# Kernel tuning notes

Hardware: AMD Instinct MI355X
Metric: run time of the kernel (lower is better)

Reference implementation:

```python
import jax, jax.numpy as jnp
import numpy as np

S = 16; N = 32768; E = 131072


def _lstm(x, h, c, Wih, Whh, b):
    # PyTorch LSTMCell: gates ordered i, f, g, o
    g = x @ Wih + h @ Whh + b
    i, f, gg, o = jnp.split(g, 4, axis=-1)
    c2 = jax.nn.sigmoid(f) * c + jax.nn.sigmoid(i) * jnp.tanh(gg)
    return jax.nn.sigmoid(o) * jnp.tanh(c2), c2


def setup_inputs() -> dict:
    key = jax.random.key(0)
    ks = jax.random.split(key, 24)
    rn = lambda k, shp, fan: (jax.random.normal(k, shp, jnp.float32) / np.float32(np.sqrt(fan)))
    return {
        'data_nodes': jax.random.normal(ks[0], (S + 1, N, 1), jnp.float32),
        'data_temporalEdges': jax.random.normal(ks[1], (S + 1, N, 2), jnp.float32),
        'data_spatialEdges': jax.random.normal(ks[2], (S + 1, E, 2), jnp.float32),
        'h_nodeRNN': jnp.zeros((N, 128), jnp.float32),
        'c_nodeRNN': jnp.zeros((N, 128), jnp.float32),
        'h_temporalEdgeRNN': jnp.zeros((N, 64), jnp.float32),
        'c_temporalEdgeRNN': jnp.zeros((N, 64), jnp.float32),
        'h_spatialEdgeRNN': jnp.zeros((E, 64), jnp.float32),
        'c_spatialEdgeRNN': jnp.zeros((E, 64), jnp.float32),
        'inc_nodes': jax.random.randint(ks[3], (2 * E,), 0, N),
        't_enc_w': rn(ks[4], (2, 64), 2), 't_enc_b': jnp.zeros((64,), jnp.float32),
        't_Wih': rn(ks[5], (64, 256), 64), 't_Whh': rn(ks[6], (64, 256), 64), 't_b': jnp.zeros((256,), jnp.float32),
        's_enc_w': rn(ks[7], (2, 64), 2), 's_enc_b': jnp.zeros((64,), jnp.float32),
        's_Wih': rn(ks[8], (64, 256), 64), 's_Whh': rn(ks[9], (64, 256), 64), 's_b': jnp.zeros((256,), jnp.float32),
        'n_enc_w': rn(ks[10], (1, 64), 1), 'n_enc_b': jnp.zeros((64,), jnp.float32),
        'ee_w': rn(ks[11], (128, 64), 128), 'ee_b': jnp.zeros((64,), jnp.float32),
        'n_Wih': rn(ks[12], (128, 512), 128), 'n_Whh': rn(ks[13], (128, 512), 128), 'n_b': jnp.zeros((512,), jnp.float32),
        'out_w': rn(ks[14], (128, 1), 128), 'out_b': jnp.zeros((1,), jnp.float32),
    }


def reference(data_nodes, data_temporalEdges, data_spatialEdges,
              h_nodeRNN, c_nodeRNN, h_temporalEdgeRNN, c_temporalEdgeRNN,
              h_spatialEdgeRNN, c_spatialEdgeRNN, inc_nodes,
              t_enc_w, t_enc_b, t_Wih, t_Whh, t_b,
              s_enc_w, s_enc_b, s_Wih, s_Whh, s_b,
              n_enc_w, n_enc_b, ee_w, ee_b, n_Wih, n_Whh, n_b, out_w, out_b):
    n_nodes = h_nodeRNN.shape[0]
    n_edges = h_spatialEdgeRNN.shape[0]
    seq_len = data_nodes.shape[0] - 1
    edge_of_inc = jnp.repeat(jnp.arange(n_edges), 2)  # edge index per incidence

    def step(carry, xs):
        ht, ct, hs, cs, hn, cn = carry
        xt, xsp, xn = xs
        # temporal EdgeRNN (dropout is identity in eval)
        ht, ct = _lstm(jax.nn.relu(xt @ t_enc_w + t_enc_b), ht, ct, t_Wih, t_Whh, t_b)
        # spatial EdgeRNN
        hs, cs = _lstm(jax.nn.relu(xsp @ s_enc_w + s_enc_b), hs, cs, s_Wih, s_Whh, s_b)
        # per-node sum of connected spatial-edge hidden states (segment reduce)
        agg = jax.ops.segment_sum(hs[edge_of_inc], inc_nodes, num_segments=n_nodes)
        h_edge = jnp.concatenate([ht, agg], axis=1)  # [N, 2*edge_rnn]
        # NodeRNN
        enc = jax.nn.relu(xn @ n_enc_w + n_enc_b)
        emb = jax.nn.relu(h_edge @ ee_w + ee_b)
        hn, cn = _lstm(jnp.concatenate([enc, emb], axis=1), hn, cn, n_Wih, n_Whh, n_b)
        out = hn @ out_w + out_b
        return (ht, ct, hs, cs, hn, cn), out

    xs = (data_temporalEdges[:seq_len], data_spatialEdges[:seq_len], data_nodes[:seq_len])
    carry0 = (h_temporalEdgeRNN, c_temporalEdgeRNN, h_spatialEdgeRNN, c_spatialEdgeRNN, h_nodeRNN, c_nodeRNN)
    _, outputs = jax.lax.scan(step, carry0, xs)
    return outputs  # [seq_len, N, node_output_size]
```

## Files before the change

### kernel.cpp

```cpp
#include <hip/hip_runtime.h>
#include <math.h>


#define S_LEN 16
#define NN 32768
#define EE 131072

typedef _Float16 f16;
typedef _Float16 f16x8 __attribute__((ext_vector_type(8)));
typedef float f32x4 __attribute__((ext_vector_type(4)));

__device__ __forceinline__ float fsigmoid(float x) {
    return __builtin_amdgcn_rcpf(1.0f + __builtin_amdgcn_exp2f(-1.44269504f * x));
}
__device__ __forceinline__ float ftanh(float x) {
    const float e = __builtin_amdgcn_exp2f(2.88539008f * x);
    return 1.0f - 2.0f * __builtin_amdgcn_rcpf(e + 1.0f);
}

__device__ __forceinline__ unsigned int pk2(float a, float b) {
    union { f16 h[2]; unsigned int u; } x;
    x.h[0] = (f16)a; x.h[1] = (f16)b;
    return x.u;
}

__device__ __forceinline__ f16x8 ld_frag16(const void* p) {
    union { uint4 v; f16x8 f; } x;
    x.v = *(const uint4*)p;
    return x.f;
}

#define CSWZ(rl) (((((rl) >> 2) & 3) ^ ((rl) & 3)) << 4)

__global__ __launch_bounds__(256) void edge_mega(
    const float* __restrict__ xT, const float* __restrict__ xS,
    const float* __restrict__ t_enc_w, const float* __restrict__ t_enc_b,
    const float* __restrict__ s_enc_w, const float* __restrict__ s_enc_b,
    const f16* __restrict__ WtT, const f16* __restrict__ WtS,
    const float* __restrict__ biasT, const float* __restrict__ biasS,
    f16* __restrict__ htAll, f16* __restrict__ hsAll,
    const float* __restrict__ cInT, const float* __restrict__ cInS,
    float* __restrict__ cOutT, float* __restrict__ cOutS,
    const int nsteps, const int writeC)
{
    constexpr int H = 64, K = 128, KSTEPS = 4, ROWB = 256, TR = 64;
    constexpr int RTN = TR / 16;
    __shared__ __align__(16) char Xls[TR * ROWB];
    __shared__ __align__(16) float cls[TR * H];
    __shared__ __align__(16) f16 hnx[TR * H];

    const int bT = NN / TR;
    const bool isT = (int)blockIdx.x < bT;
    const int row0 = (isT ? blockIdx.x : blockIdx.x - bT) * TR;
    const float* xbase = isT ? xT : xS;
    const size_t xstep = (size_t)(isT ? NN : EE) * 2;
    const float* enc_w = isT ? t_enc_w : s_enc_w;
    const float* enc_b = isT ? t_enc_b : s_enc_b;
    const f16*   Wt    = isT ? WtT : WtS;
    const float* bias  = isT ? biasT : biasS;
    f16* hAll = isT ? htAll : hsAll;
    const size_t hstep = (size_t)(isT ? NN : EE) * 64;
    const float* cIn  = (isT ? cInT : cInS) + (size_t)row0 * H;
    float*       cOut = (isT ? cOutT : cOutS) + (size_t)row0 * H;

    const int t = threadIdx.x;
    const int wv = t >> 6, l = t & 63;
    const int lane15 = l & 15, kgrp = l >> 4;
    const int col = wv * 16 + lane15;

    f16x8 bfrag[4][KSTEPS];
    #pragma unroll
    for (int q = 0; q < 4; ++q) {
        const int colq = q * H + col;
        const f16* bp = Wt + (size_t)colq * K + kgrp * 8;
        #pragma unroll
        for (int ks = 0; ks < KSTEPS; ++ks)
            bfrag[q][ks] = ld_frag16(bp + ks * 32);
    }

    for (int i = t; i < TR * H; i += 256) {
        const int r = i >> 6, j = i & 63;
        cls[(r << 6) + (j ^ CSWZ(r))] = cIn[i];
    }
    {
        const f16* hInit = hAll + (size_t)(nsteps - 1) * hstep + (size_t)row0 * H;
        for (int i = t; i < TR * (H / 4); i += 256) {
            const int r = i / (H / 4), j4 = (i % (H / 4)) * 4;
            const uint2 v = *(const uint2*)&hInit[(size_t)r * H + j4];
            const int byte = r * ROWB + ((H * 2 + j4 * 2) ^ ((r & 7) << 4));
            *(uint2*)(Xls + byte) = v;
        }
    }

    const float bi = bias[0 * H + col];
    const float bf = bias[1 * H + col];
    const float bg = bias[2 * H + col];
    const float bo = bias[3 * H + col];

    float xr0[8], xr1[8];
    {
        const float* xf = xbase;
        #pragma unroll
        for (int k2 = 0; k2 < 8; ++k2) {
            const int r = (t + k2 * 256) >> 5;
            xr0[k2] = xf[(size_t)(row0 + r) * 2 + 0];
            xr1[k2] = xf[(size_t)(row0 + r) * 2 + 1];
        }
    }

    for (int s = 0; s < nsteps; ++s) {
        #pragma unroll
        for (int k2 = 0; k2 < 8; ++k2) {
            const int i = t + k2 * 256;
            const int r = i >> 5, j2 = (i & 31) * 2;
            const float x0 = xr0[k2];
            const float x1 = xr1[k2];
            const float e0 = fmaxf(0.f, fmaf(x0, enc_w[j2],     fmaf(x1, enc_w[H + j2],     enc_b[j2])));
            const float e1 = fmaxf(0.f, fmaf(x0, enc_w[j2 + 1], fmaf(x1, enc_w[H + j2 + 1], enc_b[j2 + 1])));
            const int byte = r * ROWB + ((j2 * 2) ^ ((r & 7) << 4));
            *(unsigned int*)(Xls + byte) = pk2(e0, e1);
        }
        __syncthreads();

        if (s + 1 < nsteps) {
            const float* xf = xbase + (size_t)(s + 1) * xstep;
            #pragma unroll
            for (int k2 = 0; k2 < 8; ++k2) {
                const int r = (t + k2 * 256) >> 5;
                xr0[k2] = xf[(size_t)(row0 + r) * 2 + 0];
                xr1[k2] = xf[(size_t)(row0 + r) * 2 + 1];
            }
        }

        #pragma unroll
        for (int rt = 0; rt < RTN; ++rt) {
            const int arow = rt * 16 + lane15;
            const char* abase = Xls + arow * ROWB;
            f16x8 afrag[KSTEPS];
            #pragma unroll
            for (int ks = 0; ks < KSTEPS; ++ks) {
                const int byte = (ks * 64 + kgrp * 16) ^ ((arow & 7) << 4);
                afrag[ks] = ld_frag16(abase + byte);
            }
            f32x4 acc[4];
            #pragma unroll
            for (int q = 0; q < 4; ++q)
                #pragma unroll
                for (int r = 0; r < 4; ++r) acc[q][r] = 0.f;
            #pragma unroll
            for (int ks = 0; ks < KSTEPS; ++ks)
                #pragma unroll
                for (int q = 0; q < 4; ++q)
                    acc[q] = __builtin_amdgcn_mfma_f32_16x16x32_f16(
                        afrag[ks], bfrag[q][ks], acc[q], 0, 0, 0);
            #pragma unroll
            for (int reg = 0; reg < 4; ++reg) {
                const int rl = rt * 16 + kgrp * 4 + reg;
                const int sc = (rl << 6) + (col ^ CSWZ(rl));
                const float ig = fsigmoid(acc[0][reg] + bi);
                const float fg = fsigmoid(acc[1][reg] + bf);
                const float gg = ftanh(acc[2][reg] + bg);
                const float og = fsigmoid(acc[3][reg] + bo);
                const float c2 = fmaf(fg, cls[sc], ig * gg);
                cls[sc] = c2;
                hnx[sc] = (f16)(og * ftanh(c2));
            }
        }
        __syncthreads();

        f16* hOut = hAll + (size_t)s * hstep + (size_t)row0 * H;
        for (int i = t; i < TR * (H / 4); i += 256) {
            const int r = i / (H / 4), j4 = (i % (H / 4)) * 4;
            const uint2 v = *(const uint2*)&hnx[(r << 6) + (j4 ^ CSWZ(r))];
            *(uint2*)&hOut[(size_t)r * H + j4] = v;
            const int byte = r * ROWB + ((H * 2 + j4 * 2) ^ ((r & 7) << 4));
            *(uint2*)(Xls + byte) = v;
        }
    }

    if (writeC) {
        for (int i = t; i < TR * H; i += 256) {
            const int r = i >> 6, j = i & 63;
            cOut[i] = cls[(r << 6) + (j ^ CSWZ(r))];
        }
    }
}

__global__ __launch_bounds__(256) void gather_embed(
    const float* __restrict__ xn,
    const f16* __restrict__ ht, const f16* __restrict__ hs,
    const int* __restrict__ ptr, const int* __restrict__ rowidx,
    const float* __restrict__ n_enc_w, const float* __restrict__ n_enc_b,
    const f16* __restrict__ Wt_ee2,
    const float* __restrict__ ee_b,
    f16* __restrict__ xnode)
{
    constexpr int TR = 64, K = 192, KSTEPS = 6, ROWB = 384;
    __shared__ __align__(16) char Xls[TR * ROWB];
    const int row0 = blockIdx.x * TR;
    const int t = threadIdx.x;
    const int wv = t >> 6, l = t & 63;
    const int lane15 = l & 15, kgrp = l >> 4;

    const int col = wv * 16 + lane15;
    f16x8 bfrag[KSTEPS];
    {
        const f16* bp = Wt_ee2 + (size_t)col * K + kgrp * 8;
        #pragma unroll
        for (int ks = 0; ks < KSTEPS; ++ks) bfrag[ks] = ld_frag16(bp + ks * 32);
    }

    for (int i = t; i < TR * 16; i += 256) {
        const int r = i / 16, j4 = (i % 16) * 4;
        const uint2 v = *(const uint2*)&ht[(size_t)(row0 + r) * 64 + j4];
        const int byte = r * ROWB + ((j4 * 2) ^ ((r & 7) << 4));
        *(uint2*)(Xls + byte) = v;
    }

    {
        const int r = t >> 2, q = t & 3;
        const int n = row0 + r;
        const int beg = ptr[n], end = ptr[n + 1];
        const unsigned int* hs32 = (const unsigned int*)hs;
        float acc[16];
        #pragma unroll
        for (int j = 0; j < 16; ++j) acc[j] = 0.f;
        for (int i = beg; i < end; ++i) {
            const int e = rowidx[i];
            const unsigned int* ep = hs32 + (size_t)e * 32 + q * 8;
            #pragma unroll
            for (int j = 0; j < 8; ++j) {
                union { unsigned int u; f16 h[2]; } v;
                v.u = ep[j];
                acc[2 * j]     += (float)v.h[0];
                acc[2 * j + 1] += (float)v.h[1];
            }
        }
        #pragma unroll
        for (int j = 0; j < 8; ++j) {
            const float a0 = acc[2 * j], a1 = acc[2 * j + 1];
            const f16 h0 = (f16)a0, h1 = (f16)a1;
            const f16 l0 = (f16)(a0 - (float)h0), l1 = (f16)(a1 - (float)h1);
            union { f16 h[2]; unsigned int u; } hi, lo;
            hi.h[0] = h0; hi.h[1] = h1;
            lo.h[0] = l0; lo.h[1] = l1;
            const int bhi = r * ROWB + ((128 + q * 32 + j * 4) ^ ((r & 7) << 4));
            const int blo = r * ROWB + ((256 + q * 32 + j * 4) ^ ((r & 7) << 4));
            *(unsigned int*)(Xls + bhi) = hi.u;
            *(unsigned int*)(Xls + blo) = lo.u;
        }
    }
    __syncthreads();

    const float bb = ee_b[col];
    #pragma unroll
    for (int rt = 0; rt < TR / 16; ++rt) {
        const int arow = rt * 16 + lane15;
        const char* abase = Xls + arow * ROWB;
        f16x8 afrag[KSTEPS];
        #pragma unroll
        for (int ks = 0; ks < KSTEPS; ++ks) {
            const int byte = (ks * 64 + kgrp * 16) ^ ((arow & 7) << 4);
            afrag[ks] = ld_frag16(abase + byte);
        }
        f32x4 acc;
        #pragma unroll
        for (int r = 0; r < 4; ++r) acc[r] = 0.f;
        #pragma unroll
        for (int ks = 0; ks < KSTEPS; ++ks)
            acc = __builtin_amdgcn_mfma_f32_16x16x32_f16(afrag[ks], bfrag[ks], acc, 0, 0, 0);
        #pragma unroll
        for (int reg = 0; reg < 4; ++reg) {
            const int grow = row0 + rt * 16 + kgrp * 4 + reg;
            xnode[(size_t)grow * 128 + 64 + col] = (f16)fmaxf(0.f, acc[reg] + bb);
        }
    }

    for (int i = t; i < TR * 32; i += 256) {
        const int r = i >> 5, j2 = (i & 31) * 2;
        const int grow = row0 + r;
        const float x = xn[grow];
        const float e0 = fmaxf(0.f, fmaf(x, n_enc_w[j2],     n_enc_b[j2]));
        const float e1 = fmaxf(0.f, fmaf(x, n_enc_w[j2 + 1], n_enc_b[j2 + 1]));
        *(unsigned int*)&xnode[(size_t)grow * 128 + j2] = pk2(e0, e1);
    }
}

__global__ __launch_bounds__(512) void node_mega(
    const f16* __restrict__ xnode0,
    const f16* __restrict__ hsAllBase,
    const f16* __restrict__ Wt,
    const float* __restrict__ bias,
    const float* __restrict__ out_w, const float* __restrict__ out_b,
    f16* __restrict__ hIO,
    float* __restrict__ c,
    float* __restrict__ outp,
    const int nsteps)
{
    constexpr int H = 128, K = 256, KSTEPS = 8, ROWB = 512, TR = 128;
    constexpr int RTN = TR / 16;
    __shared__ __align__(16) char Xls[TR * ROWB];
    __shared__ __align__(16) float clsN[TR * H];
    __shared__ float out_part[TR][8];

    const int row0 = blockIdx.x * TR;
    const int t = threadIdx.x;
    const int wv = t >> 6, l = t & 63;
    const int lane15 = l & 15, kgrp = l >> 4;
    const int col = wv * 16 + lane15;

    f16x8 bfrag[4][KSTEPS];
    #pragma unroll
    for (int q = 0; q < 4; ++q) {
        const int colq = q * H + col;
        const f16* bp = Wt + (size_t)colq * K + kgrp * 8;
        #pragma unroll
        for (int ks = 0; ks < KSTEPS; ++ks)
            bfrag[q][ks] = ld_frag16(bp + ks * 32);
    }

    for (int i = t; i < TR * (H / 4); i += 512) {
        const int r = i >> 5, j4 = (i & 31) * 4;
        const uint2 v = *(const uint2*)&hIO[(size_t)(row0 + r) * H + j4];
        const int byte = r * ROWB + ((H * 2 + j4 * 2) ^ ((r & 7) << 4));
        *(uint2*)(Xls + byte) = v;
        const float4 cv = *(const float4*)&c[(size_t)(row0 + r) * H + j4];
        *(float4*)&clsN[r * H + (j4 ^ CSWZ(r))] = cv;
    }

    const float bi = bias[0 * H + col];
    const float bf = bias[1 * H + col];
    const float bg = bias[2 * H + col];
    const float bo = bias[3 * H + col];
    const float wout = out_w[col];

    for (int s = 0; s < nsteps; ++s) {
        const f16* xin = (s == 0) ? xnode0
                                  : (hsAllBase + (size_t)(s - 1) * EE * 64);
        for (int i = t; i < TR * (H / 4); i += 512) {
            const int r = i >> 5, j4 = (i & 31) * 4;
            const uint2 v = *(const uint2*)&xin[(size_t)(row0 + r) * H + j4];
            const int byte = r * ROWB + ((j4 * 2) ^ ((r & 7) << 4));
            *(uint2*)(Xls + byte) = v;
        }
        __syncthreads();

        const bool lastStep = (s == nsteps - 1);
        #pragma unroll 1
        for (int rt = 0; rt < RTN; ++rt) {
            const int arow = rt * 16 + lane15;
            const char* abase = Xls + arow * ROWB;
            f16x8 afrag[KSTEPS];
            #pragma unroll
            for (int ks = 0; ks < KSTEPS; ++ks) {
                const int byte = (ks * 64 + kgrp * 16) ^ ((arow & 7) << 4);
                afrag[ks] = ld_frag16(abase + byte);
            }
            __syncthreads();
            f32x4 acc[4];
            #pragma unroll
            for (int q = 0; q < 4; ++q)
                #pragma unroll
                for (int r = 0; r < 4; ++r) acc[q][r] = 0.f;
            #pragma unroll
            for (int ks = 0; ks < KSTEPS; ++ks)
                #pragma unroll
                for (int q = 0; q < 4; ++q)
                    acc[q] = __builtin_amdgcn_mfma_f32_16x16x32_f16(
                        afrag[ks], bfrag[q][ks], acc[q], 0, 0, 0);
            #pragma unroll
            for (int reg = 0; reg < 4; ++reg) {
                const int rl = rt * 16 + kgrp * 4 + reg;
                const int grow = row0 + rl;
                const size_t off = (size_t)grow * H + col;
                const int scn = rl * H + (col ^ CSWZ(rl));
                const float ig = fsigmoid(acc[0][reg] + bi);
                const float fg = fsigmoid(acc[1][reg] + bf);
                const float gg = ftanh(acc[2][reg] + bg);
                const float og = fsigmoid(acc[3][reg] + bo);
                const float c2 = fmaf(fg, clsN[scn], ig * gg);
                const float h2 = og * ftanh(c2);
                clsN[scn] = c2;
                const f16 h16 = (f16)h2;
                const int hbyte = rl * ROWB + ((2 * (H + col)) ^ ((rl & 7) << 4));
                *(f16*)(Xls + hbyte) = h16;
                if (lastStep) hIO[off] = h16;
                float pv = h2 * wout;
                pv += __shfl_xor(pv, 1);
                pv += __shfl_xor(pv, 2);
                pv += __shfl_xor(pv, 4);
                pv += __shfl_xor(pv, 8);
                if (lane15 == 0) out_part[rl][wv] = pv;
            }
        }
        __syncthreads();
        if (t < TR) {
            float sum = out_part[t][0];
            #pragma unroll
            for (int w = 1; w < 8; ++w) sum += out_part[t][w];
            outp[(size_t)s * NN + row0 + t] = sum + out_b[0];
        }
    }

    for (int i = t; i < TR * (H / 4); i += 512) {
        const int r = i >> 5, j4 = (i & 31) * 4;
        *(float4*)&c[(size_t)(row0 + r) * H + j4] =
            *(const float4*)&clsN[r * H + (j4 ^ CSWZ(r))];
    }
}

__global__ __launch_bounds__(256) void count_kernel(
    const int* __restrict__ inc, int* __restrict__ cnt)
{
    const int slot = blockIdx.x * 256 + threadIdx.x;
    atomicAdd(&cnt[inc[slot]], 1);
}

__global__ __launch_bounds__(1024) void scan_kernel(
    const int* __restrict__ cnt, int* __restrict__ ptr)
{
    __shared__ int sums[1024];
    const int t = threadIdx.x;
    const int base = t * 32;
    int local[32];
    int s = 0;
    #pragma unroll
    for (int i = 0; i < 32; ++i) { local[i] = s; s += cnt[base + i]; }
    sums[t] = s;
    __syncthreads();
    for (int off = 1; off < 1024; off <<= 1) {
        int v = 0;
        if (t >= off) v = sums[t - off];
        __syncthreads();
        sums[t] += v;
        __syncthreads();
    }
    const int excl = sums[t] - s;
    #pragma unroll
    for (int i = 0; i < 32; ++i) ptr[base + i] = excl + local[i];
    if (t == 1023) ptr[NN] = sums[1023];
}

__global__ __launch_bounds__(256) void fill_kernel(
    const int* __restrict__ inc, const int* __restrict__ ptr,
    int* __restrict__ cur, int* __restrict__ rowidx)
{
    const int slot = blockIdx.x * 256 + threadIdx.x;
    const int n = inc[slot];
    const int pos = atomicAdd(&cur[n], 1);
    rowidx[ptr[n] + pos] = slot >> 1;
}

__global__ __launch_bounds__(256) void sort_csr_kernel(
    const int* __restrict__ ptr, int* __restrict__ rowidx)
{
    const int n = blockIdx.x * 256 + threadIdx.x;
    if (n >= NN) return;
    const int beg = ptr[n], end = ptr[n + 1];
    for (int i = beg; i < end - 1; ++i) {
        int mi = i, mv = rowidx[i];
        for (int j = i + 1; j < end; ++j) {
            const int v = rowidx[j];
            if (v < mv) { mv = v; mi = j; }
        }
        if (mi != i) { rowidx[mi] = rowidx[i]; rowidx[i] = mv; }
    }
}

__global__ __launch_bounds__(256) void transpose_w_kernel(
    const float* __restrict__ Wih, const float* __restrict__ Whh,
    f16* __restrict__ dst, int Hk, int K, int fourH)
{
    const int tid = blockIdx.x * 256 + threadIdx.x;
    if (tid >= K * fourH) return;
    const int col = tid / K, k = tid % K;
    const float v = (k < Hk) ? Wih[(size_t)k * fourH + col]
                             : Whh[(size_t)(k - Hk) * fourH + col];
    dst[tid] = (f16)v;
}

__global__ __launch_bounds__(256) void transpose_ee2_kernel(
    const float* __restrict__ ee_w, f16* __restrict__ dst)
{
    const int tid = blockIdx.x * 256 + threadIdx.x;
    if (tid >= 64 * 192) return;
    const int col = tid / 192, k = tid % 192;
    const int srcrow = (k < 128) ? k : (k - 64);
    dst[tid] = (f16)ee_w[(size_t)srcrow * 64 + col];
}

__global__ __launch_bounds__(256) void cvt_kernel(
    const float* __restrict__ src, f16* __restrict__ dst, int n2)
{
    const int i = blockIdx.x * 256 + threadIdx.x;
    if (i >= n2) return;
    const float2 v = ((const float2*)src)[i];
    ((unsigned int*)dst)[i] = pk2(v.x, v.y);
}

extern "C" void kernel_launch(void* const* d_in, const int* in_sizes, int n_in,
                              void* d_out, int out_size, void* d_ws, size_t ws_size,
                              hipStream_t stream) {
    const float* data_nodes = (const float*)d_in[0];
    const float* data_tE    = (const float*)d_in[1];
    const float* data_sE    = (const float*)d_in[2];
    const float* h_n0 = (const float*)d_in[3];
    const float* c_n0 = (const float*)d_in[4];
    const float* h_t0 = (const float*)d_in[5];
    const float* c_t0 = (const float*)d_in[6];
    const float* h_s0 = (const float*)d_in[7];
    const float* c_s0 = (const float*)d_in[8];
    const int*   inc  = (const int*)d_in[9];
    const float* t_enc_w = (const float*)d_in[10];
    const float* t_enc_b = (const float*)d_in[11];
    const float* t_Wih   = (const float*)d_in[12];
    const float* t_Whh   = (const float*)d_in[13];
    const float* t_b     = (const float*)d_in[14];
    const float* s_enc_w = (const float*)d_in[15];
    const float* s_enc_b = (const float*)d_in[16];
    const float* s_Wih   = (const float*)d_in[17];
    const float* s_Whh   = (const float*)d_in[18];
    const float* s_b     = (const float*)d_in[19];
    const float* n_enc_w = (const float*)d_in[20];
    const float* n_enc_b = (const float*)d_in[21];
    const float* ee_w    = (const float*)d_in[22];
    const float* ee_b    = (const float*)d_in[23];
    const float* n_Wih   = (const float*)d_in[24];
    const float* n_Whh   = (const float*)d_in[25];
    const float* n_b     = (const float*)d_in[26];
    const float* out_w   = (const float*)d_in[27];
    const float* out_b   = (const float*)d_in[28];
    float* out = (float*)d_out;

    const size_t slotT = (size_t)NN * 64 * 2;
    const size_t slotS = (size_t)EE * 64 * 2;
    const size_t fixedB =
        (size_t)NN * 128 * 2 +
        (size_t)NN * 128 * 2 +
        (size_t)NN * 128 * 4 +
        (size_t)NN * 64 * 4 +
        (size_t)EE * 64 * 4 +
        ((size_t)256 * 128 + 256 * 128 + 512 * 256 + 64 * 192) * 2 +
        ((size_t)(NN + 8) + 2 * (size_t)EE + NN + NN) * 4 +
        65536;
    int CH = 16;
    while (CH > 1 && fixedB + (size_t)CH * (slotT + slotS) > ws_size) CH >>= 1;

    char* p = (char*)d_ws;
    f16*  htAll   = (f16*)p;  p += (size_t)CH * slotT;
    f16*  hsAll   = (f16*)p;  p += (size_t)CH * slotS;
    f16*  X0      = (f16*)p;  p += (size_t)NN * 128 * 2;
    f16*  hn16    = (f16*)p;  p += (size_t)NN * 128 * 2;
    float* cn     = (float*)p; p += (size_t)NN * 128 * 4;
    float* ct     = (float*)p; p += (size_t)NN * 64 * 4;
    float* cs     = (float*)p; p += (size_t)EE * 64 * 4;
    f16*  Wt_t    = (f16*)p;  p += (size_t)256 * 128 * 2;
    f16*  Wt_s    = (f16*)p;  p += (size_t)256 * 128 * 2;
    f16*  Wt_n    = (f16*)p;  p += (size_t)512 * 256 * 2;
    f16*  Wt_ee2  = (f16*)p;  p += (size_t)64 * 192 * 2;
    int*  csr_ptr = (int*)p;  p += (size_t)(NN + 8) * 4;
    int*  csr_row = (int*)p;  p += (size_t)2 * EE * 4;
    int*  cnt     = (int*)p;  p += (size_t)NN * 4;
    int*  cur     = (int*)p;  p += (size_t)NN * 4;

    cvt_kernel<<<(NN * 64 / 2 + 255) / 256, 256, 0, stream>>>(
        h_t0, htAll + (size_t)(CH - 1) * NN * 64, NN * 64 / 2);
    cvt_kernel<<<(EE * 64 / 2 + 255) / 256, 256, 0, stream>>>(
        h_s0, hsAll + (size_t)(CH - 1) * EE * 64, EE * 64 / 2);
    cvt_kernel<<<(NN * 128 / 2 + 255) / 256, 256, 0, stream>>>(h_n0, hn16, NN * 128 / 2);
    hipMemcpyAsync(cn, c_n0, (size_t)NN * 128 * 4, hipMemcpyDeviceToDevice, stream);

    transpose_w_kernel<<<(256 * 128 + 255) / 256, 256, 0, stream>>>(t_Wih, t_Whh, Wt_t, 64, 128, 256);
    transpose_w_kernel<<<(256 * 128 + 255) / 256, 256, 0, stream>>>(s_Wih, s_Whh, Wt_s, 64, 128, 256);
    transpose_w_kernel<<<(512 * 256 + 255) / 256, 256, 0, stream>>>(n_Wih, n_Whh, Wt_n, 128, 256, 512);
    transpose_ee2_kernel<<<(64 * 192 + 255) / 256, 256, 0, stream>>>(ee_w, Wt_ee2);

    hipMemsetAsync(cnt, 0, NN * sizeof(int), stream);
    hipMemsetAsync(cur, 0, NN * sizeof(int), stream);
    count_kernel<<<(2 * EE) / 256, 256, 0, stream>>>(inc, cnt);
    scan_kernel<<<1, 1024, 0, stream>>>(cnt, csr_ptr);
    fill_kernel<<<(2 * EE) / 256, 256, 0, stream>>>(inc, csr_ptr, cur, csr_row);
    sort_csr_kernel<<<NN / 256, 256, 0, stream>>>(csr_ptr, csr_row);

    const int edgeGrid = NN / 64 + EE / 64;

    for (int c0 = 0; c0 < S_LEN; c0 += CH) {
        edge_mega<<<edgeGrid, 256, 0, stream>>>(
            data_tE + (size_t)c0 * NN * 2, data_sE + (size_t)c0 * EE * 2,
            t_enc_w, t_enc_b, s_enc_w, s_enc_b,
            Wt_t, Wt_s, t_b, s_b,
            htAll, hsAll,
            (c0 == 0) ? c_t0 : ct, (c0 == 0) ? c_s0 : cs, ct, cs,
            CH, (c0 + CH < S_LEN) ? 1 : 0);

        for (int k2 = 0; k2 < CH; ++k2) {
            const int st = c0 + k2;
            f16* xnode_s = (k2 == 0) ? X0 : (hsAll + (size_t)(k2 - 1) * EE * 64);
            gather_embed<<<NN / 64, 256, 0, stream>>>(
                data_nodes + (size_t)st * NN,
                htAll + (size_t)k2 * NN * 64, hsAll + (size_t)k2 * EE * 64,
                csr_ptr, csr_row, n_enc_w, n_enc_b, Wt_ee2, ee_b, xnode_s);
        }

        node_mega<<<NN / 128, 512, 0, stream>>>(
            X0, hsAll, Wt_n, n_b, out_w, out_b, hn16, cn,
            out + (size_t)c0 * NN, CH);
    }
}
```

Before: 1.070 ms.

## Prefetch next-step node input into registers and load ht fragments directly

In the node LSTM kernel, the next step's input tile is now prefetched into registers while the current step computes, and written to LDS at the start of the next iteration. This hides global load latency behind MFMA work, at the cost of eight extra uint2 registers per thread. In gather_embed, the ht part of the A operand is read straight from global memory into MFMA fragments instead of being staged in LDS. That shrinks the LDS row from 384 to 256 bytes and removes a staging loop.

```diff
diff --git a/kernel.cpp b/kernel.cpp
--- a/kernel.cpp
+++ b/kernel.cpp
@@ -195,7 +195,7 @@
     const float* __restrict__ ee_b,
     f16* __restrict__ xnode)
 {
-    constexpr int TR = 64, K = 192, KSTEPS = 6, ROWB = 384;
+    constexpr int TR = 64, K = 192, KSTEPS = 6, ROWB = 256;
     __shared__ __align__(16) char Xls[TR * ROWB];
     const int row0 = blockIdx.x * TR;
     const int t = threadIdx.x;
@@ -208,13 +208,6 @@
         const f16* bp = Wt_ee2 + (size_t)col * K + kgrp * 8;
         #pragma unroll
         for (int ks = 0; ks < KSTEPS; ++ks) bfrag[ks] = ld_frag16(bp + ks * 32);
-    }
-
-    for (int i = t; i < TR * 16; i += 256) {
-        const int r = i / 16, j4 = (i % 16) * 4;
-        const uint2 v = *(const uint2*)&ht[(size_t)(row0 + r) * 64 + j4];
-        const int byte = r * ROWB + ((j4 * 2) ^ ((r & 7) << 4));
-        *(uint2*)(Xls + byte) = v;
     }
 
     {
@@ -244,8 +237,8 @@
             union { f16 h[2]; unsigned int u; } hi, lo;
             hi.h[0] = h0; hi.h[1] = h1;
             lo.h[0] = l0; lo.h[1] = l1;
-            const int bhi = r * ROWB + ((128 + q * 32 + j * 4) ^ ((r & 7) << 4));
-            const int blo = r * ROWB + ((256 + q * 32 + j * 4) ^ ((r & 7) << 4));
+            const int bhi = r * ROWB + ((q * 32 + j * 4) ^ ((r & 7) << 4));
+            const int blo = r * ROWB + ((128 + q * 32 + j * 4) ^ ((r & 7) << 4));
             *(unsigned int*)(Xls + bhi) = hi.u;
             *(unsigned int*)(Xls + blo) = lo.u;
         }
@@ -258,9 +251,11 @@
         const int arow = rt * 16 + lane15;
         const char* abase = Xls + arow * ROWB;
         f16x8 afrag[KSTEPS];
-        #pragma unroll
-        for (int ks = 0; ks < KSTEPS; ++ks) {
-            const int byte = (ks * 64 + kgrp * 16) ^ ((arow & 7) << 4);
+        afrag[0] = ld_frag16(&ht[(size_t)(row0 + arow) * 64 + kgrp * 8]);
+        afrag[1] = ld_frag16(&ht[(size_t)(row0 + arow) * 64 + 32 + kgrp * 8]);
+        #pragma unroll
+        for (int ks = 2; ks < KSTEPS; ++ks) {
+            const int byte = (((ks - 2) * 64) + kgrp * 16) ^ ((arow & 7) << 4);
             afrag[ks] = ld_frag16(abase + byte);
         }
         f32x4 acc;
@@ -334,14 +329,32 @@
     const float bo = bias[3 * H + col];
     const float wout = out_w[col];
 
+    uint2 xpr[8];
+    {
+        #pragma unroll
+        for (int k2 = 0; k2 < 8; ++k2) {
+            const int i = t + k2 * 512;
+            const int r = i >> 5, j4 = (i & 31) * 4;
+            xpr[k2] = *(const uint2*)&xnode0[(size_t)(row0 + r) * H + j4];
+        }
+    }
+
     for (int s = 0; s < nsteps; ++s) {
-        const f16* xin = (s == 0) ? xnode0
-                                  : (hsAllBase + (size_t)(s - 1) * EE * 64);
-        for (int i = t; i < TR * (H / 4); i += 512) {
+        #pragma unroll
+        for (int k2 = 0; k2 < 8; ++k2) {
+            const int i = t + k2 * 512;
             const int r = i >> 5, j4 = (i & 31) * 4;
-            const uint2 v = *(const uint2*)&xin[(size_t)(row0 + r) * H + j4];
             const int byte = r * ROWB + ((j4 * 2) ^ ((r & 7) << 4));
-            *(uint2*)(Xls + byte) = v;
+            *(uint2*)(Xls + byte) = xpr[k2];
+        }
+        if (s + 1 < nsteps) {
+            const f16* xin = hsAllBase + (size_t)s * EE * 64;
+            #pragma unroll
+            for (int k2 = 0; k2 < 8; ++k2) {
+                const int i = t + k2 * 512;
+                const int r = i >> 5, j4 = (i & 31) * 4;
+                xpr[k2] = *(const uint2*)&xin[(size_t)(row0 + r) * H + j4];
+            }
         }
         __syncthreads();
 
```

New measurement: 1.065 ms. About the same (-0.5%).

## Batch gather-embed across steps into one launch and move node encoding into node kernel

Applied to the files above, without the earlier changes.

Replaces the per-step gather_embed launches with a single grid covering all steps of a chunk. Each block now writes its 64-wide edge embedding in place over the temporal hidden slot instead of a separate 128-wide xnode buffer. The node input encoding (relu of xn*w+b) is computed inside node_mega rather than written and re-read from global memory. A separate htCarry buffer keeps the last temporal hidden state, since the ht slots are now overwritten. This cuts launch count and global traffic, at the cost of more parallel gather work contending for the same hs data.

```diff
diff --git a/kernel.cpp b/kernel.cpp
--- a/kernel.cpp
+++ b/kernel.cpp
@@ -39,6 +39,7 @@
     const f16* __restrict__ WtT, const f16* __restrict__ WtS,
     const float* __restrict__ biasT, const float* __restrict__ biasS,
     f16* __restrict__ htAll, f16* __restrict__ hsAll,
+    f16* __restrict__ htCarry,
     const float* __restrict__ cInT, const float* __restrict__ cInS,
     float* __restrict__ cOutT, float* __restrict__ cOutS,
     const int nsteps, const int writeC)
@@ -83,7 +84,8 @@
         cls[(r << 6) + (j ^ CSWZ(r))] = cIn[i];
     }
     {
-        const f16* hInit = hAll + (size_t)(nsteps - 1) * hstep + (size_t)row0 * H;
+        const f16* hInit = isT ? (htCarry + (size_t)row0 * H)
+                               : (hAll + (size_t)(nsteps - 1) * hstep + (size_t)row0 * H);
         for (int i = t; i < TR * (H / 4); i += 256) {
             const int r = i / (H / 4), j4 = (i % (H / 4)) * 4;
             const uint2 v = *(const uint2*)&hInit[(size_t)r * H + j4];
@@ -169,10 +171,12 @@
         __syncthreads();
 
         f16* hOut = hAll + (size_t)s * hstep + (size_t)row0 * H;
+        const bool carry = isT && (s == nsteps - 1);
         for (int i = t; i < TR * (H / 4); i += 256) {
             const int r = i / (H / 4), j4 = (i % (H / 4)) * 4;
             const uint2 v = *(const uint2*)&hnx[(r << 6) + (j4 ^ CSWZ(r))];
             *(uint2*)&hOut[(size_t)r * H + j4] = v;
+            if (carry) *(uint2*)&htCarry[(size_t)(row0 + r) * H + j4] = v;
             const int byte = r * ROWB + ((H * 2 + j4 * 2) ^ ((r & 7) << 4));
             *(uint2*)(Xls + byte) = v;
         }
@@ -186,23 +190,25 @@
     }
 }
 
-__global__ __launch_bounds__(256) void gather_embed(
-    const float* __restrict__ xn,
-    const f16* __restrict__ ht, const f16* __restrict__ hs,
+__global__ __launch_bounds__(256) void gather_embed_mega(
+    const f16* __restrict__ htAll, const f16* __restrict__ hsAll,
     const int* __restrict__ ptr, const int* __restrict__ rowidx,
-    const float* __restrict__ n_enc_w, const float* __restrict__ n_enc_b,
     const f16* __restrict__ Wt_ee2,
-    const float* __restrict__ ee_b,
-    f16* __restrict__ xnode)
-{
-    constexpr int TR = 64, K = 192, KSTEPS = 6, ROWB = 384;
+    const float* __restrict__ ee_b)
+{
+    constexpr int TR = 64, K = 192, KSTEPS = 6, ROWB = 256;
     __shared__ __align__(16) char Xls[TR * ROWB];
-    const int row0 = blockIdx.x * TR;
+    const int k2    = blockIdx.x >> 9;
+    const int panel = blockIdx.x & 511;
+    const int row0 = panel * TR;
+    f16* htSlot = (f16*)htAll + (size_t)k2 * NN * 64;
+    const f16* hsSlot = hsAll + (size_t)k2 * EE * 64;
+
     const int t = threadIdx.x;
     const int wv = t >> 6, l = t & 63;
     const int lane15 = l & 15, kgrp = l >> 4;
-
     const int col = wv * 16 + lane15;
+
     f16x8 bfrag[KSTEPS];
     {
         const f16* bp = Wt_ee2 + (size_t)col * K + kgrp * 8;
@@ -210,18 +216,19 @@
         for (int ks = 0; ks < KSTEPS; ++ks) bfrag[ks] = ld_frag16(bp + ks * 32);
     }
 
-    for (int i = t; i < TR * 16; i += 256) {
-        const int r = i / 16, j4 = (i % 16) * 4;
-        const uint2 v = *(const uint2*)&ht[(size_t)(row0 + r) * 64 + j4];
-        const int byte = r * ROWB + ((j4 * 2) ^ ((r & 7) << 4));
-        *(uint2*)(Xls + byte) = v;
+    f16x8 af0[4], af1[4];
+    #pragma unroll
+    for (int rt = 0; rt < 4; ++rt) {
+        const int arow = rt * 16 + lane15;
+        af0[rt] = ld_frag16(&htSlot[(size_t)(row0 + arow) * 64 + kgrp * 8]);
+        af1[rt] = ld_frag16(&htSlot[(size_t)(row0 + arow) * 64 + 32 + kgrp * 8]);
     }
 
     {
         const int r = t >> 2, q = t & 3;
         const int n = row0 + r;
         const int beg = ptr[n], end = ptr[n + 1];
-        const unsigned int* hs32 = (const unsigned int*)hs;
+        const unsigned int* hs32 = (const unsigned int*)hsSlot;
         float acc[16];
         #pragma unroll
         for (int j = 0; j < 16; ++j) acc[j] = 0.f;
@@ -244,8 +251,8 @@
             union { f16 h[2]; unsigned int u; } hi, lo;
             hi.h[0] = h0; hi.h[1] = h1;
             lo.h[0] = l0; lo.h[1] = l1;
-            const int bhi = r * ROWB + ((128 + q * 32 + j * 4) ^ ((r & 7) << 4));
-            const int blo = r * ROWB + ((256 + q * 32 + j * 4) ^ ((r & 7) << 4));
+            const int bhi = r * ROWB + ((q * 32 + j * 4) ^ ((r & 7) << 4));
+            const int blo = r * ROWB + ((128 + q * 32 + j * 4) ^ ((r & 7) << 4));
             *(unsigned int*)(Xls + bhi) = hi.u;
             *(unsigned int*)(Xls + blo) = lo.u;
         }
@@ -258,9 +265,11 @@
         const int arow = rt * 16 + lane15;
         const char* abase = Xls + arow * ROWB;
         f16x8 afrag[KSTEPS];
-        #pragma unroll
-        for (int ks = 0; ks < KSTEPS; ++ks) {
-            const int byte = (ks * 64 + kgrp * 16) ^ ((arow & 7) << 4);
+        afrag[0] = af0[rt];
+        afrag[1] = af1[rt];
+        #pragma unroll
+        for (int ks = 2; ks < KSTEPS; ++ks) {
+            const int byte = (((ks - 2) * 64) + kgrp * 16) ^ ((arow & 7) << 4);
             afrag[ks] = ld_frag16(abase + byte);
         }
         f32x4 acc;
@@ -272,25 +281,17 @@
         #pragma unroll
         for (int reg = 0; reg < 4; ++reg) {
             const int grow = row0 + rt * 16 + kgrp * 4 + reg;
-            xnode[(size_t)grow * 128 + 64 + col] = (f16)fmaxf(0.f, acc[reg] + bb);
-        }
-    }
-
-    for (int i = t; i < TR * 32; i += 256) {
-        const int r = i >> 5, j2 = (i & 31) * 2;
-        const int grow = row0 + r;
-        const float x = xn[grow];
-        const float e0 = fmaxf(0.f, fmaf(x, n_enc_w[j2],     n_enc_b[j2]));
-        const float e1 = fmaxf(0.f, fmaf(x, n_enc_w[j2 + 1], n_enc_b[j2 + 1]));
-        *(unsigned int*)&xnode[(size_t)grow * 128 + j2] = pk2(e0, e1);
+            htSlot[(size_t)grow * 64 + col] = (f16)fmaxf(0.f, acc[reg] + bb);
+        }
     }
 }
 
 __global__ __launch_bounds__(512) void node_mega(
-    const f16* __restrict__ xnode0,
-    const f16* __restrict__ hsAllBase,
+    const float* __restrict__ xnBase,
+    const f16* __restrict__ embAll,
     const f16* __restrict__ Wt,
     const float* __restrict__ bias,
+    const float* __restrict__ n_enc_w, const float* __restrict__ n_enc_b,
     const float* __restrict__ out_w, const float* __restrict__ out_b,
     f16* __restrict__ hIO,
     float* __restrict__ c,
@@ -335,12 +336,20 @@
     const float wout = out_w[col];
 
     for (int s = 0; s < nsteps; ++s) {
-        const f16* xin = (s == 0) ? xnode0
-                                  : (hsAllBase + (size_t)(s - 1) * EE * 64);
-        for (int i = t; i < TR * (H / 4); i += 512) {
-            const int r = i >> 5, j4 = (i & 31) * 4;
-            const uint2 v = *(const uint2*)&xin[(size_t)(row0 + r) * H + j4];
-            const int byte = r * ROWB + ((j4 * 2) ^ ((r & 7) << 4));
+        const float* xn = xnBase + (size_t)s * NN;
+        for (int i = t; i < TR * 32; i += 512) {
+            const int r = i >> 5, j2 = (i & 31) * 2;
+            const float x = xn[row0 + r];
+            const float e0 = fmaxf(0.f, fmaf(x, n_enc_w[j2],     n_enc_b[j2]));
+            const float e1 = fmaxf(0.f, fmaf(x, n_enc_w[j2 + 1], n_enc_b[j2 + 1]));
+            const int byte = r * ROWB + ((j2 * 2) ^ ((r & 7) << 4));
+            *(unsigned int*)(Xls + byte) = pk2(e0, e1);
+        }
+        const f16* emb = embAll + (size_t)s * NN * 64;
+        for (int i = t; i < TR * 16; i += 512) {
+            const int r = i >> 4, j4 = (i & 15) * 4;
+            const uint2 v = *(const uint2*)&emb[(size_t)(row0 + r) * 64 + j4];
+            const int byte = r * ROWB + ((2 * (64 + j4)) ^ ((r & 7) << 4));
             *(uint2*)(Xls + byte) = v;
         }
         __syncthreads();
@@ -535,7 +544,7 @@
     const size_t slotT = (size_t)NN * 64 * 2;
     const size_t slotS = (size_t)EE * 64 * 2;
     const size_t fixedB =
-        (size_t)NN * 128 * 2 +
+        (size_t)NN * 64 * 2 +
         (size_t)NN * 128 * 2 +
         (size_t)NN * 128 * 4 +
         (size_t)NN * 64 * 4 +
@@ -549,7 +558,7 @@
     char* p = (char*)d_ws;
     f16*  htAll   = (f16*)p;  p += (size_t)CH * slotT;
     f16*  hsAll   = (f16*)p;  p += (size_t)CH * slotS;
-    f16*  X0      = (f16*)p;  p += (size_t)NN * 128 * 2;
+    f16*  htCarry = (f16*)p;  p += (size_t)NN * 64 * 2;
     f16*  hn16    = (f16*)p;  p += (size_t)NN * 128 * 2;
     float* cn     = (float*)p; p += (size_t)NN * 128 * 4;
     float* ct     = (float*)p; p += (size_t)NN * 64 * 4;
@@ -563,8 +572,7 @@
     int*  cnt     = (int*)p;  p += (size_t)NN * 4;
     int*  cur     = (int*)p;  p += (size_t)NN * 4;
 
-    cvt_kernel<<<(NN * 64 / 2 + 255) / 256, 256, 0, stream>>>(
-        h_t0, htAll + (size_t)(CH - 1) * NN * 64, NN * 64 / 2);
+    cvt_kernel<<<(NN * 64 / 2 + 255) / 256, 256, 0, stream>>>(h_t0, htCarry, NN * 64 / 2);
     cvt_kernel<<<(EE * 64 / 2 + 255) / 256, 256, 0, stream>>>(
         h_s0, hsAll + (size_t)(CH - 1) * EE * 64, EE * 64 / 2);
     cvt_kernel<<<(NN * 128 / 2 + 255) / 256, 256, 0, stream>>>(h_n0, hn16, NN * 128 / 2);
@@ -589,21 +597,16 @@
             data_tE + (size_t)c0 * NN * 2, data_sE + (size_t)c0 * EE * 2,
             t_enc_w, t_enc_b, s_enc_w, s_enc_b,
             Wt_t, Wt_s, t_b, s_b,
-            htAll, hsAll,
+            htAll, hsAll, htCarry,
             (c0 == 0) ? c_t0 : ct, (c0 == 0) ? c_s0 : cs, ct, cs,
             CH, (c0 + CH < S_LEN) ? 1 : 0);
 
-        for (int k2 = 0; k2 < CH; ++k2) {
-            const int st = c0 + k2;
-            f16* xnode_s = (k2 == 0) ? X0 : (hsAll + (size_t)(k2 - 1) * EE * 64);
-            gather_embed<<<NN / 64, 256, 0, stream>>>(
-                data_nodes + (size_t)st * NN,
-                htAll + (size_t)k2 * NN * 64, hsAll + (size_t)k2 * EE * 64,
-                csr_ptr, csr_row, n_enc_w, n_enc_b, Wt_ee2, ee_b, xnode_s);
-        }
+        gather_embed_mega<<<CH * (NN / 64), 256, 0, stream>>>(
+            htAll, hsAll, csr_ptr, csr_row, Wt_ee2, ee_b);
 
         node_mega<<<NN / 128, 512, 0, stream>>>(
-            X0, hsAll, Wt_n, n_b, out_w, out_b, hn16, cn,
+            data_nodes + (size_t)c0 * NN, htAll, Wt_n, n_b,
+            n_enc_w, n_enc_b, out_w, out_b, hn16, cn,
             out + (size_t)c0 * NN, CH);
     }
 }
```

Measured after the change: 933.0 us (median of 2 runs). -12.8%, faster.
